# Kernel optimization log

Measured on AMD Instinct MI355X. Metric: run time of the kernel, lower is better.

## Reference

```python
import jax, jax.numpy as jnp
import numpy as np

N, M = 2048, 256
INPUT_DIM, EMBED_DIM, HIDDEN = 512, 256, 512


def setup_inputs() -> dict:
    key = jax.random.key(0)
    ks = jax.random.split(key, 12)
    s = 0.02
    inp = {
        "x": jax.random.normal(ks[0], (N, INPUT_DIM), dtype=jnp.float32),
        "tuples": jax.random.randint(ks[1], (M, 3), 0, 8, dtype=jnp.int64),
        # x_net: Linear(input_dim, hidden) -> ReLU -> Linear(hidden, embed_dim) -> ReLU
        "Wa": s * jax.random.normal(ks[2], (HIDDEN, INPUT_DIM), dtype=jnp.float32),
        "ba": jnp.zeros((HIDDEN,), dtype=jnp.float32),
        "Wb": s * jax.random.normal(ks[3], (EMBED_DIM, HIDDEN), dtype=jnp.float32),
        "bb": jnp.zeros((EMBED_DIM,), dtype=jnp.float32),
        # embedding tables
        "E_pred": s * jax.random.normal(ks[4], (8, EMBED_DIM), dtype=jnp.float32),
        "E_filt": s * jax.random.normal(ks[5], (192, EMBED_DIM), dtype=jnp.float32),
        "E_reo": s * jax.random.normal(ks[6], (8, EMBED_DIM), dtype=jnp.float32),
        # mlp: Linear(2*embed_dim, hidden) -> ReLU -> Linear(hidden, 1)
        "W1": s * jax.random.normal(ks[7], (HIDDEN, 2 * EMBED_DIM), dtype=jnp.float32),
        "b1": jnp.zeros((HIDDEN,), dtype=jnp.float32),
        "W2": s * jax.random.normal(ks[8], (1, HIDDEN), dtype=jnp.float32),
        "b2": jnp.zeros((1,), dtype=jnp.float32),
    }
    return inp


def reference(x, tuples, Wa, ba, Wb, bb, E_pred, E_filt, E_reo, W1, b1, W2, b2):
    # x_net: two Linear+ReLU layers -> x_emb [N, D]
    h_x = jax.nn.relu(jnp.einsum('ni,hi->nh', x, Wa) + ba)
    x_emb = jax.nn.relu(jnp.einsum('nh,dh->nd', h_x, Wb) + bb)
    # tuple embedding sum -> t_emb [M, D]
    t_emb = E_pred[tuples[:, 0]] + E_filt[tuples[:, 1]] + E_reo[tuples[:, 2]]
    # mlp first layer on concat([x_exp, t_exp]) == Wx @ x_emb + Wt @ t_emb (split W1)
    D = x_emb.shape[1]
    W1x, W1t = W1[:, :D], W1[:, D:]
    hx = jnp.einsum('nd,hd->nh', x_emb, W1x)          # [N, H]
    ht = jnp.einsum('md,hd->mh', t_emb, W1t)          # [M, H]
    h = jax.nn.relu(hx[:, None, :] + ht[None, :, :] + b1)  # [N, M, H]
    out = jnp.einsum('nmh,h->nm', h, W2[0]) + b2[0]   # [N, M]
    return out
```

## Files before the change

### kernel.cpp

```cpp
#include <hip/hip_runtime.h>

constexpr int N_     = 2048;
constexpr int IN_DIM = 512;
constexpr int HID    = 512;
constexpr int EMB    = 256;
constexpr int M_     = 256;

typedef __attribute__((ext_vector_type(8))) short short8;
typedef __attribute__((ext_vector_type(4))) float f32x4;
typedef __attribute__((ext_vector_type(2))) _Float16 h2v;

#if defined(__has_builtin)
#if __has_builtin(__builtin_amdgcn_fdot2)
#define HAVE_FDOT2 1
#endif
#endif

union U32H2 { unsigned int u; h2v v; };

__device__ __forceinline__ unsigned short f2bf(float f) {
    union { float f; unsigned int u; } v; v.f = f;
    return (unsigned short)((v.u + 0x7fffu + ((v.u >> 16) & 1u)) >> 16);
}
__device__ __forceinline__ unsigned int packh2(float a, float b) {
    U32H2 r; r.v[0] = (_Float16)a; r.v[1] = (_Float16)b; return r.u;
}
__device__ __forceinline__ h2v relu2(h2v s) {
#if defined(__has_builtin) && __has_builtin(__builtin_elementwise_max)
    U32H2 z; z.u = 0u;
    return __builtin_elementwise_max(s, z.v);
#else
    U32H2 t; t.v = s;
    const unsigned int m = ((t.u & 0x80000000u) ? 0xFFFF0000u : 0u) |
                           ((t.u & 0x00008000u) ? 0x0000FFFFu : 0u);
    t.u &= ~m;
    return t.v;
#endif
}

__global__ __launch_bounds__(256)
void prep(const float* __restrict__ x, const float* __restrict__ Wa,
          const float* __restrict__ Wb, const float* __restrict__ W1,
          const int* __restrict__ tuples, const float* __restrict__ Ep,
          const float* __restrict__ Ef, const float* __restrict__ Er,
          const float* __restrict__ w2,
          unsigned short* __restrict__ x_bf, unsigned short* __restrict__ Wa_bf,
          unsigned short* __restrict__ Wb_bf, unsigned short* __restrict__ W1x_bf,
          unsigned short* __restrict__ W1t_bf, unsigned short* __restrict__ t_emb_bf,
          unsigned int* __restrict__ w2p)
{
    const int b = blockIdx.x, t = threadIdx.x;
    if (b < 1664) {
        int q = b * 256 + t;
        float4 v; ushort4 u;
        if (q < 262144) {
            v = ((const float4*)x)[q];
            u.x = f2bf(v.x); u.y = f2bf(v.y); u.z = f2bf(v.z); u.w = f2bf(v.w);
            ((ushort4*)x_bf)[q] = u;
        } else if ((q -= 262144) < 65536) {
            v = ((const float4*)Wa)[q];
            u.x = f2bf(v.x); u.y = f2bf(v.y); u.z = f2bf(v.z); u.w = f2bf(v.w);
            ((ushort4*)Wa_bf)[q] = u;
        } else if ((q -= 65536) < 32768) {
            v = ((const float4*)Wb)[q];
            u.x = f2bf(v.x); u.y = f2bf(v.y); u.z = f2bf(v.z); u.w = f2bf(v.w);
            ((ushort4*)Wb_bf)[q] = u;
        } else {
            q -= 32768;
            v = ((const float4*)W1)[q];
            u.x = f2bf(v.x); u.y = f2bf(v.y); u.z = f2bf(v.z); u.w = f2bf(v.w);
            const int row = q >> 7, c = (q & 127) * 4;
            if (c < 256) ((ushort4*)W1x_bf)[(row * 256 + c) >> 2] = u;
            else         ((ushort4*)W1t_bf)[(row * 256 + c - 256) >> 2] = u;
        }
    } else if (b < 1728) {
        const int idx = (b - 1664) * 256 + t;
        const int m = idx >> 6, q = idx & 63;
        const int t0 = tuples[m * 3 + 0];
        const int t1 = tuples[m * 3 + 1];
        const int t2 = tuples[m * 3 + 2];
        const float4 a = ((const float4*)(Ep + t0 * EMB))[q];
        const float4 c = ((const float4*)(Ef + t1 * EMB))[q];
        const float4 d = ((const float4*)(Er + t2 * EMB))[q];
        ushort4 u;
        u.x = f2bf(a.x + c.x + d.x);
        u.y = f2bf(a.y + c.y + d.y);
        u.z = f2bf(a.z + c.z + d.z);
        u.w = f2bf(a.w + c.w + d.w);
        ((ushort4*)t_emb_bf)[m * 64 + q] = u;
    } else {
        w2p[t] = packh2(w2[2 * t], w2[2 * t + 1]);
    }
}

template<int BM, int BN, bool RELU, bool BIASC>
__global__ __launch_bounds__(256)
void gemm_bf16(const unsigned short* __restrict__ A, int lda,
               const unsigned short* __restrict__ W, int ldw,
               const float* __restrict__ bias,
               unsigned short* __restrict__ Cout, int ldc, int K)
{
    constexpr int BK = 64;
    constexpr int SM = BM / 2, SN = BN / 2;
    constexpr int FM = SM / 16, FN = SN / 16;
    constexpr int AIT = BM / 32, WIT = BN / 32;
    __shared__ unsigned short As[2][BM][BK + 8];
    __shared__ unsigned short Bs[2][BN][BK + 8];

    const int tid  = threadIdx.x;
    const int row0 = blockIdx.x * BM, col0 = blockIdx.y * BN;
    const int wv = tid >> 6, lane = tid & 63;
    const int wr = wv >> 1, wc = wv & 1;
    const int lr = lane & 15, lq = lane >> 4;

    f32x4 acc[FM][FN];
#pragma unroll
    for (int i = 0; i < FM; ++i)
#pragma unroll
        for (int j = 0; j < FN; ++j) acc[i][j] = (f32x4)0.f;

    short8 pa[AIT], pw[WIT];
    auto issue = [&](int k0) {
#pragma unroll
        for (int i = 0; i < AIT; ++i) {
            const int idx = tid + i * 256, r = idx >> 3, c8 = idx & 7;
            pa[i] = *(const short8*)&A[(size_t)(row0 + r) * lda + k0 + c8 * 8];
        }
#pragma unroll
        for (int i = 0; i < WIT; ++i) {
            const int idx = tid + i * 256, r = idx >> 3, c8 = idx & 7;
            pw[i] = *(const short8*)&W[(size_t)(col0 + r) * ldw + k0 + c8 * 8];
        }
    };
    auto store = [&](int bsel) {
#pragma unroll
        for (int i = 0; i < AIT; ++i) {
            const int idx = tid + i * 256, r = idx >> 3, c8 = idx & 7;
            *(short8*)&As[bsel][r][c8 * 8] = pa[i];
        }
#pragma unroll
        for (int i = 0; i < WIT; ++i) {
            const int idx = tid + i * 256, r = idx >> 3, c8 = idx & 7;
            *(short8*)&Bs[bsel][r][c8 * 8] = pw[i];
        }
    };

    issue(0); store(0);
    const int NC = K / BK;
    for (int c = 0; c < NC; ++c) {
        const int buf = c & 1;
        __syncthreads();
        if (c + 1 < NC) issue((c + 1) * BK);
#pragma unroll
        for (int ks = 0; ks < 2; ++ks) {
            short8 af[FM], bfr[FN];
#pragma unroll
            for (int i = 0; i < FM; ++i)
                af[i] = *(const short8*)&As[buf][wr * SM + i * 16 + lr][ks * 32 + lq * 8];
#pragma unroll
            for (int j = 0; j < FN; ++j)
                bfr[j] = *(const short8*)&Bs[buf][wc * SN + j * 16 + lr][ks * 32 + lq * 8];
#pragma unroll
            for (int i = 0; i < FM; ++i)
#pragma unroll
                for (int j = 0; j < FN; ++j)
                    acc[i][j] = __builtin_amdgcn_mfma_f32_16x16x32_bf16(
                        af[i], bfr[j], acc[i][j], 0, 0, 0);
        }
        if (c + 1 < NC) store((c + 1) & 1);
    }

#pragma unroll
    for (int i = 0; i < FM; ++i) {
#pragma unroll
        for (int j = 0; j < FN; ++j) {
            const int colb = col0 + wc * SN + j * 16 + lr;
#pragma unroll
            for (int e = 0; e < 4; ++e) {
                const int row = row0 + wr * SM + i * 16 + lq * 4 + e;
                float v = acc[i][j][e];
                if (BIASC) v += bias[colb];
                if (RELU)  v = fmaxf(v, 0.f);
                Cout[(size_t)row * ldc + colb] = f2bf(v);
            }
        }
    }
}

__global__ __launch_bounds__(256)
void gemm_pair(const unsigned short* __restrict__ W1x_bf,
               const unsigned short* __restrict__ W1t_bf,
               const unsigned short* __restrict__ x_emb_bf,
               const unsigned short* __restrict__ t_emb_bf,
               const float* __restrict__ b1,
               unsigned int* __restrict__ hxT_p,
               unsigned int* __restrict__ cmT_p)
{
    constexpr int BM = 32, BN = 64, BK = 64;
    constexpr int SM = 16, SN = 32, FN = 2;
    __shared__ unsigned short As[2][BM][BK + 8];
    __shared__ unsigned short Bs[2][BN][BK + 8];

    const unsigned short* A; const unsigned short* B;
    const float* bias; unsigned int* outp; int ldc, col0;
    if (blockIdx.y < 32) {
        A = W1x_bf; B = x_emb_bf; bias = nullptr; outp = hxT_p;
        ldc = N_; col0 = blockIdx.y * BN;
    } else {
        A = W1t_bf; B = t_emb_bf; bias = b1; outp = cmT_p;
        ldc = M_; col0 = (blockIdx.y - 32) * BN;
    }
    const int K = EMB, row0 = blockIdx.x * BM;

    const int tid = threadIdx.x;
    const int wv = tid >> 6, lane = tid & 63;
    const int wr = wv >> 1, wc = wv & 1;
    const int lr = lane & 15, lq = lane >> 4;

    f32x4 acc[FN];
#pragma unroll
    for (int j = 0; j < FN; ++j) acc[j] = (f32x4)0.f;

    short8 pa, pw[2];
    auto issue = [&](int k0) {
        { const int r = tid >> 3, c8 = tid & 7;
          pa = *(const short8*)&A[(size_t)(row0 + r) * K + k0 + c8 * 8]; }
#pragma unroll
        for (int i = 0; i < 2; ++i) {
            const int idx = tid + i * 256, r = idx >> 3, c8 = idx & 7;
            pw[i] = *(const short8*)&B[(size_t)(col0 + r) * K + k0 + c8 * 8];
        }
    };
    auto store = [&](int bsel) {
        { const int r = tid >> 3, c8 = tid & 7;
          *(short8*)&As[bsel][r][c8 * 8] = pa; }
#pragma unroll
        for (int i = 0; i < 2; ++i) {
            const int idx = tid + i * 256, r = idx >> 3, c8 = idx & 7;
            *(short8*)&Bs[bsel][r][c8 * 8] = pw[i];
        }
    };

    issue(0); store(0);
    const int NC = K / BK;
    for (int c = 0; c < NC; ++c) {
        const int buf = c & 1;
        __syncthreads();
        if (c + 1 < NC) issue((c + 1) * BK);
#pragma unroll
        for (int ks = 0; ks < 2; ++ks) {
            short8 af, bfr[FN];
            af = *(const short8*)&As[buf][wr * SM + lr][ks * 32 + lq * 8];
#pragma unroll
            for (int j = 0; j < FN; ++j)
                bfr[j] = *(const short8*)&Bs[buf][wc * SN + j * 16 + lr][ks * 32 + lq * 8];
#pragma unroll
            for (int j = 0; j < FN; ++j)
                acc[j] = __builtin_amdgcn_mfma_f32_16x16x32_bf16(
                    af, bfr[j], acc[j], 0, 0, 0);
        }
        if (c + 1 < NC) store((c + 1) & 1);
    }

    const int rowb = row0 + wr * SM + lq * 4;
#pragma unroll
    for (int j = 0; j < FN; ++j) {
        const int colb = col0 + wc * SN + j * 16 + lr;
#pragma unroll
        for (int e2 = 0; e2 < 2; ++e2) {
            float v0 = acc[j][2 * e2], v1 = acc[j][2 * e2 + 1];
            if (bias) { v0 += bias[rowb + 2 * e2]; v1 += bias[rowb + 2 * e2 + 1]; }
            outp[(size_t)((rowb >> 1) + e2) * ldc + colb] = packh2(v0, v1);
        }
    }
}

__global__ __launch_bounds__(256, 2)
void fused_out(const unsigned int* __restrict__ hxT_p,
               const unsigned int* __restrict__ cmT_p,
               const unsigned int* __restrict__ w2p,
               unsigned int* __restrict__ part_u32)
{
    constexpr int TN = 64, TM = 64, H2B = 64;
    __shared__ unsigned int Hs[H2B][TN + 4];
    __shared__ unsigned int Cs[H2B][TM + 4];
    __shared__ unsigned int Wsh[H2B];

    const int tid = threadIdx.x;
    const int tx = tid & 15, ty = tid >> 4;
    const int n0 = blockIdx.x * TN;
    const int m0 = blockIdx.y * TM;
    const int kb = blockIdx.z * H2B;

#pragma unroll
    for (int p = 0; p < 4; ++p) {
        const int idx = tid + p * 256, r = idx >> 4, c4 = idx & 15;
        *(uint4*)&Hs[r][c4 * 4] =
            *(const uint4*)&hxT_p[(size_t)(kb + r) * N_ + n0 + c4 * 4];
        *(uint4*)&Cs[r][c4 * 4] =
            *(const uint4*)&cmT_p[(size_t)(kb + r) * M_ + m0 + c4 * 4];
    }
    if (tid < H2B) Wsh[tid] = w2p[kb + tid];
    __syncthreads();

    float acc[4][4];
#pragma unroll
    for (int i = 0; i < 4; ++i)
#pragma unroll
        for (int j = 0; j < 4; ++j) acc[i][j] = 0.f;

#ifdef HAVE_FDOT2
#pragma unroll 8
    for (int h = 0; h < H2B; ++h) {
        const uint4 av = *(const uint4*)&Hs[h][ty * 4];
        const uint4 bv = *(const uint4*)&Cs[h][tx * 4];
        U32H2 w; w.u = Wsh[h];
        U32H2 a[4], b[4];
        a[0].u = av.x; a[1].u = av.y; a[2].u = av.z; a[3].u = av.w;
        b[0].u = bv.x; b[1].u = bv.y; b[2].u = bv.z; b[3].u = bv.w;
#pragma unroll
        for (int i = 0; i < 4; ++i)
#pragma unroll
            for (int j = 0; j < 4; ++j) {
                const h2v s = relu2(a[i].v + b[j].v);
                acc[i][j] = __builtin_amdgcn_fdot2(s, w.v, acc[i][j], false);
            }
    }
#else
    U32H2 facc[4][4];
#pragma unroll
    for (int i = 0; i < 4; ++i)
#pragma unroll
        for (int j = 0; j < 4; ++j) facc[i][j].u = 0u;
#pragma unroll
    for (int hb = 0; hb < H2B / 8; ++hb) {
#pragma unroll
        for (int hh = 0; hh < 8; ++hh) {
            const int h = hb * 8 + hh;
            const uint4 av = *(const uint4*)&Hs[h][ty * 4];
            const uint4 bv = *(const uint4*)&Cs[h][tx * 4];
            U32H2 w; w.u = Wsh[h];
            U32H2 a[4], b[4];
            a[0].u = av.x; a[1].u = av.y; a[2].u = av.z; a[3].u = av.w;
            b[0].u = bv.x; b[1].u = bv.y; b[2].u = bv.z; b[3].u = bv.w;
#pragma unroll
            for (int i = 0; i < 4; ++i)
#pragma unroll
                for (int j = 0; j < 4; ++j) {
                    const h2v s = relu2(a[i].v + b[j].v);
                    facc[i][j].v = s * w.v + facc[i][j].v;
                }
        }
#pragma unroll
        for (int i = 0; i < 4; ++i)
#pragma unroll
            for (int j = 0; j < 4; ++j) {
                acc[i][j] += (float)facc[i][j].v[0] + (float)facc[i][j].v[1];
                facc[i][j].u = 0u;
            }
    }
#endif

#pragma unroll
    for (int i = 0; i < 4; ++i) {
        const int n = n0 + ty * 4 + i;
        const size_t base = ((size_t)blockIdx.z * N_ + n) * (M_ / 2) + (m0 >> 1) + tx * 2;
        part_u32[base]     = packh2(acc[i][0], acc[i][1]);
        part_u32[base + 1] = packh2(acc[i][2], acc[i][3]);
    }
}

__global__ __launch_bounds__(256)
void reduce_out(const unsigned short* __restrict__ part,
                const float* __restrict__ b2,
                float* __restrict__ out)
{
    const int g = blockIdx.x * 256 + threadIdx.x;
    const int n = g >> 5;
    const int m0 = (g & 31) * 8;
    const float bb = b2[0];
    float s[8];
#pragma unroll
    for (int i = 0; i < 8; ++i) s[i] = bb;
#pragma unroll
    for (int zz = 0; zz < 4; ++zz) {
        const uint4 v = *(const uint4*)&part[((size_t)zz * N_ + n) * M_ + m0];
        const unsigned int vv[4] = {v.x, v.y, v.z, v.w};
#pragma unroll
        for (int q = 0; q < 4; ++q) {
            U32H2 u; u.u = vv[q];
            s[2 * q]     += (float)u.v[0];
            s[2 * q + 1] += (float)u.v[1];
        }
    }
    float4 o0 = {s[0], s[1], s[2], s[3]};
    float4 o1 = {s[4], s[5], s[6], s[7]};
    *(float4*)&out[(size_t)n * M_ + m0]     = o0;
    *(float4*)&out[(size_t)n * M_ + m0 + 4] = o1;
}

extern "C" void kernel_launch(void* const* d_in, const int* in_sizes, int n_in,
                              void* d_out, int out_size, void* d_ws, size_t ws_size,
                              hipStream_t stream)
{
    const float* x      = (const float*)d_in[0];
    const int*   tuples = (const int*)d_in[1];
    const float* Wa     = (const float*)d_in[2];
    const float* ba     = (const float*)d_in[3];
    const float* Wb     = (const float*)d_in[4];
    const float* bb     = (const float*)d_in[5];
    const float* E_pred = (const float*)d_in[6];
    const float* E_filt = (const float*)d_in[7];
    const float* E_reo  = (const float*)d_in[8];
    const float* W1     = (const float*)d_in[9];
    const float* b1     = (const float*)d_in[10];
    const float* W2     = (const float*)d_in[11];
    const float* b2     = (const float*)d_in[12];
    float* out = (float*)d_out;

    char* w = (char*)d_ws;
    unsigned short* x_bf     = (unsigned short*)(w + 0);
    unsigned int*   hxT_p    = (unsigned int*)(w + 0);
    unsigned short* h_x_bf   = (unsigned short*)(w + 2097152);
    unsigned int*   part_u32 = (unsigned int*)(w + 2097152);
    unsigned short* x_emb_bf = (unsigned short*)(w + 4194304);
    unsigned short* Wa_bf    = (unsigned short*)(w + 5242880);
    unsigned short* Wb_bf    = (unsigned short*)(w + 5767168);
    unsigned short* W1x_bf   = (unsigned short*)(w + 6029312);
    unsigned int*   cmT_p    = (unsigned int*)(w + 6291456);
    unsigned short* W1t_bf   = (unsigned short*)(w + 6553600);
    unsigned short* t_emb_bf = (unsigned short*)(w + 6815744);
    unsigned int*   w2p      = (unsigned int*)(w + 6946816);

    prep<<<dim3(1729), dim3(256), 0, stream>>>(
        x, Wa, Wb, W1, tuples, E_pred, E_filt, E_reo, W2,
        x_bf, Wa_bf, Wb_bf, W1x_bf, W1t_bf, t_emb_bf, w2p);

    gemm_bf16<32, 64, true, true><<<dim3(N_ / 32, HID / 64), 256, 0, stream>>>(
        x_bf, IN_DIM, Wa_bf, IN_DIM, ba, h_x_bf, HID, IN_DIM);

    gemm_bf16<32, 32, true, true><<<dim3(N_ / 32, EMB / 32), 256, 0, stream>>>(
        h_x_bf, HID, Wb_bf, HID, bb, x_emb_bf, EMB, HID);

    gemm_pair<<<dim3(HID / 32, 36), 256, 0, stream>>>(
        W1x_bf, W1t_bf, x_emb_bf, t_emb_bf, b1, hxT_p, cmT_p);

    fused_out<<<dim3(N_ / 64, M_ / 64, 4), 256, 0, stream>>>(
        hxT_p, cmT_p, w2p, part_u32);

    reduce_out<<<dim3(65536 / 256), 256, 0, stream>>>(
        (const unsigned short*)part_u32, b2, out);
}
```

Measured before the change: 121.1 us.

## Replace split-K reduce kernel with atomic accumulation and enlarge GEMM K-tiles

The fused output kernel now atomically adds its fp32 partial sums (with the bias on the first z slice) straight into the zero-initialised output. This removes the separate reduce kernel and its fp16 partial-buffer round trip, at the cost of a memset and 4-way atomic contention per element. Separately, the bf16 GEMMs move to a K-tile of 128 and get a min-2-blocks launch bound. That halves the barrier count per GEMM but raises LDS use and register pressure.

```diff
diff --git a/kernel.cpp b/kernel.cpp
--- a/kernel.cpp
+++ b/kernel.cpp
@@ -94,18 +94,18 @@
 }
 
 template<int BM, int BN, bool RELU, bool BIASC>
-__global__ __launch_bounds__(256)
+__global__ __launch_bounds__(256, 2)
 void gemm_bf16(const unsigned short* __restrict__ A, int lda,
                const unsigned short* __restrict__ W, int ldw,
                const float* __restrict__ bias,
                unsigned short* __restrict__ Cout, int ldc, int K)
 {
-    constexpr int BK = 64;
+    constexpr int BK = 128, LDK = BK + 8;
     constexpr int SM = BM / 2, SN = BN / 2;
     constexpr int FM = SM / 16, FN = SN / 16;
-    constexpr int AIT = BM / 32, WIT = BN / 32;
-    __shared__ unsigned short As[2][BM][BK + 8];
-    __shared__ unsigned short Bs[2][BN][BK + 8];
+    constexpr int AIT = BM / 16, WIT = BN / 16;
+    __shared__ unsigned short As[2][BM][LDK];
+    __shared__ unsigned short Bs[2][BN][LDK];
 
     const int tid  = threadIdx.x;
     const int row0 = blockIdx.x * BM, col0 = blockIdx.y * BN;
@@ -123,24 +123,24 @@
     auto issue = [&](int k0) {
 #pragma unroll
         for (int i = 0; i < AIT; ++i) {
-            const int idx = tid + i * 256, r = idx >> 3, c8 = idx & 7;
+            const int idx = tid + i * 256, r = idx >> 4, c8 = idx & 15;
             pa[i] = *(const short8*)&A[(size_t)(row0 + r) * lda + k0 + c8 * 8];
         }
 #pragma unroll
         for (int i = 0; i < WIT; ++i) {
-            const int idx = tid + i * 256, r = idx >> 3, c8 = idx & 7;
+            const int idx = tid + i * 256, r = idx >> 4, c8 = idx & 15;
             pw[i] = *(const short8*)&W[(size_t)(col0 + r) * ldw + k0 + c8 * 8];
         }
     };
     auto store = [&](int bsel) {
 #pragma unroll
         for (int i = 0; i < AIT; ++i) {
-            const int idx = tid + i * 256, r = idx >> 3, c8 = idx & 7;
+            const int idx = tid + i * 256, r = idx >> 4, c8 = idx & 15;
             *(short8*)&As[bsel][r][c8 * 8] = pa[i];
         }
 #pragma unroll
         for (int i = 0; i < WIT; ++i) {
-            const int idx = tid + i * 256, r = idx >> 3, c8 = idx & 7;
+            const int idx = tid + i * 256, r = idx >> 4, c8 = idx & 15;
             *(short8*)&Bs[bsel][r][c8 * 8] = pw[i];
         }
     };
@@ -152,7 +152,7 @@
         __syncthreads();
         if (c + 1 < NC) issue((c + 1) * BK);
 #pragma unroll
-        for (int ks = 0; ks < 2; ++ks) {
+        for (int ks = 0; ks < BK / 32; ++ks) {
             short8 af[FM], bfr[FN];
 #pragma unroll
             for (int i = 0; i < FM; ++i)
@@ -187,7 +187,7 @@
     }
 }
 
-__global__ __launch_bounds__(256)
+__global__ __launch_bounds__(256, 2)
 void gemm_pair(const unsigned short* __restrict__ W1x_bf,
                const unsigned short* __restrict__ W1t_bf,
                const unsigned short* __restrict__ x_emb_bf,
@@ -196,10 +196,10 @@
                unsigned int* __restrict__ hxT_p,
                unsigned int* __restrict__ cmT_p)
 {
-    constexpr int BM = 32, BN = 64, BK = 64;
+    constexpr int BM = 32, BN = 64, BK = 128, LDK = BK + 8;
     constexpr int SM = 16, SN = 32, FN = 2;
-    __shared__ unsigned short As[2][BM][BK + 8];
-    __shared__ unsigned short Bs[2][BN][BK + 8];
+    __shared__ unsigned short As[2][BM][LDK];
+    __shared__ unsigned short Bs[2][BN][LDK];
 
     const unsigned short* A; const unsigned short* B;
     const float* bias; unsigned int* outp; int ldc, col0;
@@ -221,22 +221,28 @@
 #pragma unroll
     for (int j = 0; j < FN; ++j) acc[j] = (f32x4)0.f;
 
-    short8 pa, pw[2];
+    short8 pa[2], pw[4];
     auto issue = [&](int k0) {
-        { const int r = tid >> 3, c8 = tid & 7;
-          pa = *(const short8*)&A[(size_t)(row0 + r) * K + k0 + c8 * 8]; }
 #pragma unroll
         for (int i = 0; i < 2; ++i) {
-            const int idx = tid + i * 256, r = idx >> 3, c8 = idx & 7;
+            const int idx = tid + i * 256, r = idx >> 4, c8 = idx & 15;
+            pa[i] = *(const short8*)&A[(size_t)(row0 + r) * K + k0 + c8 * 8];
+        }
+#pragma unroll
+        for (int i = 0; i < 4; ++i) {
+            const int idx = tid + i * 256, r = idx >> 4, c8 = idx & 15;
             pw[i] = *(const short8*)&B[(size_t)(col0 + r) * K + k0 + c8 * 8];
         }
     };
     auto store = [&](int bsel) {
-        { const int r = tid >> 3, c8 = tid & 7;
-          *(short8*)&As[bsel][r][c8 * 8] = pa; }
 #pragma unroll
         for (int i = 0; i < 2; ++i) {
-            const int idx = tid + i * 256, r = idx >> 3, c8 = idx & 7;
+            const int idx = tid + i * 256, r = idx >> 4, c8 = idx & 15;
+            *(short8*)&As[bsel][r][c8 * 8] = pa[i];
+        }
+#pragma unroll
+        for (int i = 0; i < 4; ++i) {
+            const int idx = tid + i * 256, r = idx >> 4, c8 = idx & 15;
             *(short8*)&Bs[bsel][r][c8 * 8] = pw[i];
         }
     };
@@ -248,7 +254,7 @@
         __syncthreads();
         if (c + 1 < NC) issue((c + 1) * BK);
 #pragma unroll
-        for (int ks = 0; ks < 2; ++ks) {
+        for (int ks = 0; ks < BK / 32; ++ks) {
             short8 af, bfr[FN];
             af = *(const short8*)&As[buf][wr * SM + lr][ks * 32 + lq * 8];
 #pragma unroll
@@ -256,8 +262,7 @@
                 bfr[j] = *(const short8*)&Bs[buf][wc * SN + j * 16 + lr][ks * 32 + lq * 8];
 #pragma unroll
             for (int j = 0; j < FN; ++j)
-                acc[j] = __builtin_amdgcn_mfma_f32_16x16x32_bf16(
-                    af, bfr[j], acc[j], 0, 0, 0);
+                acc[j] = __builtin_amdgcn_mfma_f32_16x16x32_bf16(af, bfr[j], acc[j], 0, 0, 0);
         }
         if (c + 1 < NC) store((c + 1) & 1);
     }
@@ -279,11 +284,12 @@
 void fused_out(const unsigned int* __restrict__ hxT_p,
                const unsigned int* __restrict__ cmT_p,
                const unsigned int* __restrict__ w2p,
-               unsigned int* __restrict__ part_u32)
+               const float* __restrict__ b2,
+               float* __restrict__ out)
 {
-    constexpr int TN = 64, TM = 64, H2B = 64;
-    __shared__ unsigned int Hs[H2B][TN + 4];
-    __shared__ unsigned int Cs[H2B][TM + 4];
+    constexpr int TN = 64, TM = 64, H2B = 64, LDT = 68;
+    __shared__ unsigned int Hs[H2B][LDT];
+    __shared__ unsigned int Cs[H2B][LDT];
     __shared__ unsigned int Wsh[H2B];
 
     const int tid = threadIdx.x;
@@ -361,42 +367,14 @@
     }
 #endif
 
+    const float bb = (blockIdx.z == 0) ? b2[0] : 0.f;
 #pragma unroll
     for (int i = 0; i < 4; ++i) {
         const int n = n0 + ty * 4 + i;
-        const size_t base = ((size_t)blockIdx.z * N_ + n) * (M_ / 2) + (m0 >> 1) + tx * 2;
-        part_u32[base]     = packh2(acc[i][0], acc[i][1]);
-        part_u32[base + 1] = packh2(acc[i][2], acc[i][3]);
-    }
-}
-
-__global__ __launch_bounds__(256)
-void reduce_out(const unsigned short* __restrict__ part,
-                const float* __restrict__ b2,
-                float* __restrict__ out)
-{
-    const int g = blockIdx.x * 256 + threadIdx.x;
-    const int n = g >> 5;
-    const int m0 = (g & 31) * 8;
-    const float bb = b2[0];
-    float s[8];
-#pragma unroll
-    for (int i = 0; i < 8; ++i) s[i] = bb;
-#pragma unroll
-    for (int zz = 0; zz < 4; ++zz) {
-        const uint4 v = *(const uint4*)&part[((size_t)zz * N_ + n) * M_ + m0];
-        const unsigned int vv[4] = {v.x, v.y, v.z, v.w};
-#pragma unroll
-        for (int q = 0; q < 4; ++q) {
-            U32H2 u; u.u = vv[q];
-            s[2 * q]     += (float)u.v[0];
-            s[2 * q + 1] += (float)u.v[1];
-        }
-    }
-    float4 o0 = {s[0], s[1], s[2], s[3]};
-    float4 o1 = {s[4], s[5], s[6], s[7]};
-    *(float4*)&out[(size_t)n * M_ + m0]     = o0;
-    *(float4*)&out[(size_t)n * M_ + m0 + 4] = o1;
+#pragma unroll
+        for (int j = 0; j < 4; ++j)
+            atomicAdd(&out[(size_t)n * M_ + m0 + tx * 4 + j], acc[i][j] + bb);
+    }
 }
 
 extern "C" void kernel_launch(void* const* d_in, const int* in_sizes, int n_in,
@@ -422,7 +400,6 @@
     unsigned short* x_bf     = (unsigned short*)(w + 0);
     unsigned int*   hxT_p    = (unsigned int*)(w + 0);
     unsigned short* h_x_bf   = (unsigned short*)(w + 2097152);
-    unsigned int*   part_u32 = (unsigned int*)(w + 2097152);
     unsigned short* x_emb_bf = (unsigned short*)(w + 4194304);
     unsigned short* Wa_bf    = (unsigned short*)(w + 5242880);
     unsigned short* Wb_bf    = (unsigned short*)(w + 5767168);
@@ -432,6 +409,8 @@
     unsigned short* t_emb_bf = (unsigned short*)(w + 6815744);
     unsigned int*   w2p      = (unsigned int*)(w + 6946816);
 
+    hipMemsetAsync(d_out, 0, (size_t)N_ * M_ * sizeof(float), stream);
+
     prep<<<dim3(1729), dim3(256), 0, stream>>>(
         x, Wa, Wb, W1, tuples, E_pred, E_filt, E_reo, W2,
         x_bf, Wa_bf, Wb_bf, W1x_bf, W1t_bf, t_emb_bf, w2p);
@@ -446,8 +425,5 @@
         W1x_bf, W1t_bf, x_emb_bf, t_emb_bf, b1, hxT_p, cmT_p);
 
     fused_out<<<dim3(N_ / 64, M_ / 64, 4), 256, 0, stream>>>(
-        hxT_p, cmT_p, w2p, part_u32);
-
-    reduce_out<<<dim3(65536 / 256), 256, 0, stream>>>(
-        (const unsigned short*)part_u32, b2, out);
-}
+        hxT_p, cmT_p, w2p, b2, out);
+}
```

After: 139.8 us. +15.5%, slower.
